# Performance work log

Measured on AMD Instinct MI355X. Metric: run time of the kernel, lower is better.

## Reference

```python
import jax, jax.numpy as jnp
import numpy as np

N_HEAD = 12

def setup_inputs() -> dict:
    key = jax.random.key(0)
    ks = jax.random.split(key, 3)
    B, T, D = 4, 2048, 768
    x = jax.random.normal(ks[0], (B, T, D), dtype=jnp.float32)
    W_qkv = jax.random.normal(ks[1], (D, 3 * D), dtype=jnp.float32) * (1.0 / np.sqrt(D))
    b_qkv = jnp.zeros((3 * D,), dtype=jnp.float32)
    W_o = jax.random.normal(ks[2], (D, D), dtype=jnp.float32) * (1.0 / np.sqrt(D))
    b_o = jnp.zeros((D,), dtype=jnp.float32)
    return {"x": x, "W_qkv": W_qkv, "b_qkv": b_qkv, "W_o": W_o, "b_o": b_o}


def reference(x, W_qkv, b_qkv, W_o, b_o):
    B, T, D = x.shape
    H = N_HEAD
    hd = D // H
    qkv = x @ W_qkv + b_qkv                      # [B,T,3D]
    q, k, v = jnp.split(qkv, 3, axis=-1)
    # [B,T,D] -> [B,H,T,hd]
    q = q.reshape(B, T, H, hd).transpose(0, 2, 1, 3)
    k = k.reshape(B, T, H, hd).transpose(0, 2, 1, 3)
    v = v.reshape(B, T, H, hd).transpose(0, 2, 1, 3)
    scale = 1.0 / np.sqrt(hd).astype(np.float32)
    scores = jnp.einsum('bhqd,bhkd->bhqk', q, k) * scale   # [B,H,T,T]
    causal = jnp.tril(jnp.ones((T, T), dtype=bool))
    scores = jnp.where(causal[None, None, :, :], scores, -jnp.inf)
    attn = jax.nn.softmax(scores, axis=-1)
    out = jnp.einsum('bhqk,bhkd->bhqd', attn, v)            # [B,H,T,hd]
    out = out.transpose(0, 2, 1, 3).reshape(B, T, D)
    return out @ W_o + b_o
```

## Files before the change

### kernel.cpp

```cpp
#include <hip/hip_runtime.h>
#include <hip/hip_bf16.h>

typedef __bf16 bf16_t;
typedef float f32x4 __attribute__((ext_vector_type(4)));
typedef bf16_t bf16x8 __attribute__((ext_vector_type(8)));
typedef bf16_t bf16x4 __attribute__((ext_vector_type(4)));

#define MFMA16(a, b, c) __builtin_amdgcn_mfma_f32_16x16x32_bf16(a, b, c, 0, 0, 0)

#define QSCALE 0.18033688011112042f

__device__ __forceinline__ void gl_lds16(const bf16_t* g, bf16_t* l) {
    __builtin_amdgcn_global_load_lds(
        (const __attribute__((address_space(1))) unsigned int*)g,
        (__attribute__((address_space(3))) unsigned int*)l, 16, 0, 0);
}

__device__ __forceinline__ float fexp2(float x) {
    float y;
    asm("v_exp_f32 %0, %1" : "=v"(y) : "v"(x));
    return y;
}

__device__ __forceinline__ void conv_t_body(const float* __restrict__ in,
                                            bf16_t* __restrict__ out,
                                            int R, int C, int bx, int by,
                                            float (*t)[33]) {
    const int tx = threadIdx.x & 31;
    const int ty = threadIdx.x >> 5;
#pragma unroll
    for (int i = 0; i < 4; i++)
        t[ty + i * 8][tx] = in[(size_t)(by + ty + i * 8) * C + bx + tx];
    __syncthreads();
#pragma unroll
    for (int i = 0; i < 4; i++)
        out[(size_t)(bx + ty + i * 8) * R + by + tx] = (bf16_t)t[tx][ty + i * 8];
}

__global__ __launch_bounds__(256) void prep_k(
    const float* __restrict__ x,    bf16_t* __restrict__ xb,
    const float* __restrict__ Wqkv, bf16_t* __restrict__ Wt,
    const float* __restrict__ Wo,   bf16_t* __restrict__ Wot)
{
    __shared__ float t[32][33];
    const int blk = blockIdx.x;
    if (blk < 6144) {
        const int i = (blk * 256 + threadIdx.x) * 4;
        float4 v = *(const float4*)(x + i);
        bf16x4 o = { (bf16_t)v.x, (bf16_t)v.y, (bf16_t)v.z, (bf16_t)v.w };
        *(bf16x4*)(xb + i) = o;
    } else if (blk < 7872) {
        const int idx = blk - 6144;
        conv_t_body(Wqkv, Wt, 768, 2304, (idx % 72) * 32, (idx / 72) * 32, t);
    } else {
        const int idx = blk - 7872;
        conv_t_body(Wo, Wot, 768, 768, (idx % 24) * 32, (idx / 24) * 32, t);
    }
}

__global__ __launch_bounds__(256) void vtrans(const bf16_t* __restrict__ Vp,
                                              bf16_t* __restrict__ Vt) {
    __shared__ __align__(16) bf16_t Ts[64 * 72];
    const int t0 = blockIdx.x * 64;
    const int bh = blockIdx.y;
    const int r  = threadIdx.x >> 2;
    const int cb = (threadIdx.x & 3) * 16;
    const bf16_t* src = Vp + (((size_t)bh * 2048 + t0 + r) << 6) + cb;
    *(bf16x8*)(Ts + r * 72 + cb)     = *(const bf16x8*)(src);
    *(bf16x8*)(Ts + r * 72 + cb + 8) = *(const bf16x8*)(src + 8);
    __syncthreads();
    const int f  = threadIdx.x >> 2;
    const int tb = (threadIdx.x & 3) * 16;
    bf16_t* dst = Vt + (((size_t)bh * 64 + f) << 11) + t0 + tb;
    bf16x8 a, b;
#pragma unroll
    for (int i = 0; i < 8; i++) a[i] = Ts[(tb + i) * 72 + f];
#pragma unroll
    for (int i = 0; i < 8; i++) b[i] = Ts[(tb + 8 + i) * 72 + f];
    *(bf16x8*)(dst)     = a;
    *(bf16x8*)(dst + 8) = b;
}

template <int EPI>
__global__ __launch_bounds__(256) void gemm_bt(
    const bf16_t* __restrict__ A, const bf16_t* __restrict__ Bt,
    const float* __restrict__ bias,
    void* __restrict__ O0v, bf16_t* __restrict__ O1, bf16_t* __restrict__ O2,
    int M, int N, int K)
{
    __shared__ __align__(16) bf16_t As[2][128 * 32];
    __shared__ __align__(16) bf16_t Bs[2][128 * 32];

    const int tid  = threadIdx.x;
    const int wid  = tid >> 6;
    const int lane = tid & 63;
    const int quad = lane >> 4;
    const int l15  = lane & 15;
    const int wm   = (wid >> 1) * 64;
    const int wn   = (wid & 1) * 64;
    const int qs8  = (quad ^ ((l15 >> 1) & 3)) * 8;

    const int mtiles = M >> 7;
    const int mtpx   = mtiles >> 3;
    const int bid    = blockIdx.x;
    const int xcd    = bid & 7;
    const int slot   = bid >> 3;
    const int m0     = (xcd * mtpx + (slot % mtpx)) << 7;
    const int n0     = (slot / mtpx) << 7;

    f32x4 acc[4][4];
#pragma unroll
    for (int i = 0; i < 4; i++)
#pragma unroll
        for (int j = 0; j < 4; j++) acc[i][j] = (f32x4){0.f, 0.f, 0.f, 0.f};

    const int srow = tid >> 2;
    const int scol = (((tid & 3) ^ ((srow >> 1) & 3)) ) * 8;
    const bf16_t* ag0 = A  + (size_t)(m0 + srow) * K + scol;
    const bf16_t* ag1 = A  + (size_t)(m0 + 64 + srow) * K + scol;
    const bf16_t* bg0 = Bt + (size_t)(n0 + srow) * K + scol;
    const bf16_t* bg1 = Bt + (size_t)(n0 + 64 + srow) * K + scol;

    auto prefetch = [&](int k0, int buf) {
        gl_lds16(ag0 + k0, As[buf] + tid * 8);
        gl_lds16(ag1 + k0, As[buf] + 2048 + tid * 8);
        gl_lds16(bg0 + k0, Bs[buf] + tid * 8);
        gl_lds16(bg1 + k0, Bs[buf] + 2048 + tid * 8);
    };

    const int niter = K >> 5;
    prefetch(0, 0);
    for (int i = 0; i < niter; i++) {
        __syncthreads();
        if (i + 1 < niter) prefetch((i + 1) << 5, (i + 1) & 1);
        const bf16_t* Ap = As[i & 1];
        const bf16_t* Bp = Bs[i & 1];

        bf16x8 af[4], bfr[4];
#pragma unroll
        for (int ii = 0; ii < 4; ii++)
            af[ii] = *(const bf16x8*)(Ap + (wm + ii * 16 + l15) * 32 + qs8);
#pragma unroll
        for (int j = 0; j < 4; j++)
            bfr[j] = *(const bf16x8*)(Bp + (wn + j * 16 + l15) * 32 + qs8);
#pragma unroll
        for (int ii = 0; ii < 4; ii++)
#pragma unroll
            for (int j = 0; j < 4; j++)
                acc[ii][j] = MFMA16(af[ii], bfr[j], acc[ii][j]);
    }

    if (EPI == 0) {
        const int sec = n0 / 768;
        const float scale = (sec == 0) ? QSCALE : 1.f;
        bf16_t* dst = (sec == 0) ? (bf16_t*)O0v : (sec == 1 ? O1 : O2);
#pragma unroll
        for (int i = 0; i < 4; i++) {
            const int mbase = m0 + wm + i * 16 + quad * 4;
#pragma unroll
            for (int j = 0; j < 4; j++) {
                const int n  = n0 + wn + j * 16 + l15;
                const float bv = bias[n];
                const int d    = n - sec * 768;
                const int h    = d >> 6;
                const int feat = d & 63;
#pragma unroll
                for (int r = 0; r < 4; r++) {
                    const int mm = mbase + r;
                    const int b  = mm >> 11;
                    const int tt = mm & 2047;
                    const int bh = b * 12 + h;
                    dst[(((size_t)bh * 2048 + tt) << 6) + feat] =
                        (bf16_t)((acc[i][j][r] + bv) * scale);
                }
            }
        }
    } else {
#pragma unroll
        for (int i = 0; i < 4; i++) {
            const int mbase = m0 + wm + i * 16 + quad * 4;
#pragma unroll
            for (int j = 0; j < 4; j++) {
                const int n  = n0 + wn + j * 16 + l15;
                const float bv = bias[n];
#pragma unroll
                for (int r = 0; r < 4; r++)
                    ((float*)O0v)[(size_t)(mbase + r) * N + n] = acc[i][j][r] + bv;
            }
        }
    }
}

__global__ __launch_bounds__(256) void attn_k(
    const bf16_t* __restrict__ Q, const bf16_t* __restrict__ Kb,
    const bf16_t* __restrict__ Vt, bf16_t* __restrict__ AO)
{
    __shared__ __align__(16) bf16_t Ks[2 * 4096];
    __shared__ __align__(16) bf16_t Vs[2 * 4096];
    __shared__ __align__(16) bf16_t Ps[4 * 16 * 64];

    const int tid  = threadIdx.x;
    const int wid  = tid >> 6;
    const int lane = tid & 63;
    const int quad = lane >> 4;
    const int l15  = lane & 15;
    const int qs8  = (quad ^ ((l15 >> 1) & 3)) * 8;

    const int bid  = blockIdx.x;
    const int xcd  = bid & 7;
    const int slot = bid >> 3;
    const int bh   = xcd * 6 + (slot >> 4);
    const int p    = slot & 15;

    const bf16_t* Qb  = Q  + ((size_t)bh << 17);
    const bf16_t* Kbh = Kb + ((size_t)bh << 17);
    const bf16_t* Vbh = Vt + ((size_t)bh << 17);

    bf16_t* Pw = Ps + wid * 1024;
    const int swl = l15 & 7;
    bf16_t* pwr[4];
#pragma unroll
    for (int c = 0; c < 4; c++)
        pwr[c] = Pw + l15 * 64 + (((((c << 1) | (quad >> 1))) ^ swl) << 3) + ((quad & 1) << 2);
    const bf16_t* prd[2];
#pragma unroll
    for (int kk = 0; kk < 2; kk++)
        prd[kk] = Pw + l15 * 64 + ((((kk << 2) | quad) ^ swl) << 3);

    const bf16x8 ones = { (bf16_t)1.f, (bf16_t)1.f, (bf16_t)1.f, (bf16_t)1.f,
                          (bf16_t)1.f, (bf16_t)1.f, (bf16_t)1.f, (bf16_t)1.f };

    const int srow = tid >> 2;
    const int scol = (((tid & 3) ^ ((srow >> 1) & 3))) * 8;

    auto prefetch = [&](int j, int buf) {
        const int kv0 = j * 64;
        bf16_t* kd = Ks + buf * 4096 + tid * 8;
        bf16_t* vd = Vs + buf * 4096 + tid * 8;
#pragma unroll
        for (int c = 0; c < 2; c++) {
            gl_lds16(Kbh + (size_t)(kv0 + srow) * 64 + c * 32 + scol, kd + c * 2048);
            gl_lds16(Vbh + (size_t)srow * 2048 + kv0 + c * 32 + scol, vd + c * 2048);
        }
    };

    const int b = bh / 12;
    const int h = bh - b * 12;

#pragma unroll
    for (int half = 0; half < 2; half++) {
        const int qt = half == 0 ? (31 - p) : p;
        const int q0 = qt * 64;
        const int qg = q0 + wid * 16 + l15;

        bf16x8 qf[2];
        {
            const bf16_t* qp = Qb + ((size_t)qg << 6) + quad * 8;
            qf[0] = *(const bf16x8*)(qp);
            qf[1] = *(const bf16x8*)(qp + 32);
        }

        f32x4 lacc = (f32x4){0.f, 0.f, 0.f, 0.f};
        f32x4 oacc[4];
#pragma unroll
        for (int f = 0; f < 4; f++) oacc[f] = (f32x4){0.f, 0.f, 0.f, 0.f};

        const int cnt = qt + 1;
        prefetch(0, 0);

        for (int i = 0; i < cnt; i++) {
            __syncthreads();
            if (i + 1 < cnt) prefetch(i + 1, (i + 1) & 1);
            const bf16_t* Kp = Ks + (i & 1) * 4096;
            const bf16_t* Vp = Vs + (i & 1) * 4096;

            f32x4 st[4];
            __builtin_amdgcn_s_setprio(1);
#pragma unroll
            for (int c = 0; c < 4; c++) {
                st[c] = (f32x4){0.f, 0.f, 0.f, 0.f};
#pragma unroll
                for (int kk = 0; kk < 2; kk++) {
                    bf16x8 kf = *(const bf16x8*)(Kp + kk * 2048 + (c * 16 + l15) * 32 + qs8);
                    st[c] = MFMA16(kf, qf[kk], st[c]);
                }
            }
            __builtin_amdgcn_s_setprio(0);

            if (i == qt) {
                const int kvb = q0 + quad * 4;
#pragma unroll
                for (int c = 0; c < 4; c++)
#pragma unroll
                    for (int r = 0; r < 4; r++)
                        if (kvb + c * 16 + r > qg) st[c][r] = -3e38f;
            }

#pragma unroll
            for (int c = 0; c < 4; c++) {
                bf16x4 pk = { (bf16_t)fexp2(st[c][0]), (bf16_t)fexp2(st[c][1]),
                              (bf16_t)fexp2(st[c][2]), (bf16_t)fexp2(st[c][3]) };
                *(bf16x4*)pwr[c] = pk;
            }

            bf16x8 pb[2];
#pragma unroll
            for (int kk = 0; kk < 2; kk++)
                pb[kk] = *(const bf16x8*)prd[kk];

            __builtin_amdgcn_s_setprio(1);
            lacc = MFMA16(ones, pb[0], lacc);
            lacc = MFMA16(ones, pb[1], lacc);

#pragma unroll
            for (int f = 0; f < 4; f++)
#pragma unroll
                for (int kk = 0; kk < 2; kk++) {
                    bf16x8 vf = *(const bf16x8*)(Vp + kk * 2048 + (f * 16 + l15) * 32 + qs8);
                    oacc[f] = MFMA16(vf, pb[kk], oacc[f]);
                }
            __builtin_amdgcn_s_setprio(0);
        }
        __syncthreads();

        const float inv = 1.0f / lacc[0];
        bf16_t* dst = AO + ((size_t)(b * 2048 + qg)) * 768 + h * 64 + quad * 4;
#pragma unroll
        for (int f = 0; f < 4; f++) {
            bf16x4 o = { (bf16_t)(oacc[f][0] * inv), (bf16_t)(oacc[f][1] * inv),
                         (bf16_t)(oacc[f][2] * inv), (bf16_t)(oacc[f][3] * inv) };
            *(bf16x4*)(dst + f * 16) = o;
        }
    }
}

extern "C" void kernel_launch(void* const* d_in, const int* in_sizes, int n_in,
                              void* d_out, int out_size, void* d_ws, size_t ws_size,
                              hipStream_t stream)
{
    const float* x    = (const float*)d_in[0];
    const float* Wqkv = (const float*)d_in[1];
    const float* bqkv = (const float*)d_in[2];
    const float* Wo   = (const float*)d_in[3];
    const float* bo   = (const float*)d_in[4];
    float* out = (float*)d_out;

    const size_t per = (size_t)48 * 2048 * 64;
    bf16_t* Qs  = (bf16_t*)d_ws;
    bf16_t* Kk  = Qs + per;
    bf16_t* Vt  = Kk + per;
    bf16_t* AO  = Vt + per;
    bf16_t* xb  = AO + per;
    bf16_t* Wt  = xb + per;
    bf16_t* Wot = Wt + (size_t)2304 * 768;
    bf16_t* Vpl = (bf16_t*)d_out;

    prep_k<<<8448, 256, 0, stream>>>(x, xb, Wqkv, Wt, Wo, Wot);

    gemm_bt<0><<<18 * 64, 256, 0, stream>>>(
        xb, Wt, bqkv, (void*)Qs, Kk, Vpl, 8192, 2304, 768);
    vtrans<<<dim3(32, 48), 256, 0, stream>>>(Vpl, Vt);
    attn_k<<<768, 256, 0, stream>>>(Qs, Kk, Vt, AO);
    gemm_bt<1><<<6 * 64, 256, 0, stream>>>(
        AO, Wot, bo, (void*)out, nullptr, nullptr, 8192, 768, 768);
}
```

Before: 197.8 us.

## Process two 64-row query tiles per block to reuse K/V tiles

The attention kernel now gives each block a 128-row query tile, processed as two 64-row groups per warp that share every K/V tile loaded into LDS. Before, each block walked two separate 64-row tiles (a paired long and short tile) and reloaded K/V for each. The change is meant to halve LDS fills and barriers per unit of MFMA work. In exchange it doubles the accumulators and P scratch, sets launch_bounds to 3 blocks, and changes the causal work balance: block i-loop lengths now vary from 2 to 32 tiles instead of being paired to a constant total.

```diff
diff --git a/kernel.cpp b/kernel.cpp
--- a/kernel.cpp
+++ b/kernel.cpp
@@ -191,13 +191,13 @@
     }
 }
 
-__global__ __launch_bounds__(256) void attn_k(
+__global__ __launch_bounds__(256, 3) void attn_k(
     const bf16_t* __restrict__ Q, const bf16_t* __restrict__ Kb,
     const bf16_t* __restrict__ Vt, bf16_t* __restrict__ AO)
 {
     __shared__ __align__(16) bf16_t Ks[2 * 4096];
     __shared__ __align__(16) bf16_t Vs[2 * 4096];
-    __shared__ __align__(16) bf16_t Ps[4 * 16 * 64];
+    __shared__ __align__(16) bf16_t Ps[4 * 2048];
 
     const int tid  = threadIdx.x;
     const int wid  = tid >> 6;
@@ -209,23 +209,28 @@
     const int bid  = blockIdx.x;
     const int xcd  = bid & 7;
     const int slot = bid >> 3;
-    const int bh   = xcd * 6 + (slot >> 4);
-    const int p    = slot & 15;
+    const int bh   = xcd * 6 + (slot % 6);
+    const int qt2  = 15 - (slot / 6);
+    const int q0   = qt2 << 7;
 
     const bf16_t* Qb  = Q  + ((size_t)bh << 17);
     const bf16_t* Kbh = Kb + ((size_t)bh << 17);
     const bf16_t* Vbh = Vt + ((size_t)bh << 17);
 
-    bf16_t* Pw = Ps + wid * 1024;
+    bf16_t* Pw = Ps + wid * 2048;
     const int swl = l15 & 7;
-    bf16_t* pwr[4];
-#pragma unroll
-    for (int c = 0; c < 4; c++)
-        pwr[c] = Pw + l15 * 64 + (((((c << 1) | (quad >> 1))) ^ swl) << 3) + ((quad & 1) << 2);
-    const bf16_t* prd[2];
-#pragma unroll
-    for (int kk = 0; kk < 2; kk++)
-        prd[kk] = Pw + l15 * 64 + ((((kk << 2) | quad) ^ swl) << 3);
+    bf16_t* pwr[2][4];
+    const bf16_t* prd[2][2];
+#pragma unroll
+    for (int g = 0; g < 2; g++) {
+#pragma unroll
+        for (int c = 0; c < 4; c++)
+            pwr[g][c] = Pw + g * 1024 + l15 * 64 +
+                        (((((c << 1) | (quad >> 1))) ^ swl) << 3) + ((quad & 1) << 2);
+#pragma unroll
+        for (int kk = 0; kk < 2; kk++)
+            prd[g][kk] = Pw + g * 1024 + l15 * 64 + ((((kk << 2) | quad) ^ swl) << 3);
+    }
 
     const bf16x8 ones = { (bf16_t)1.f, (bf16_t)1.f, (bf16_t)1.f, (bf16_t)1.f,
                           (bf16_t)1.f, (bf16_t)1.f, (bf16_t)1.f, (bf16_t)1.f };
@@ -247,88 +252,108 @@
     const int b = bh / 12;
     const int h = bh - b * 12;
 
-#pragma unroll
-    for (int half = 0; half < 2; half++) {
-        const int qt = half == 0 ? (31 - p) : p;
-        const int q0 = qt * 64;
-        const int qg = q0 + wid * 16 + l15;
-
-        bf16x8 qf[2];
-        {
-            const bf16_t* qp = Qb + ((size_t)qg << 6) + quad * 8;
-            qf[0] = *(const bf16x8*)(qp);
-            qf[1] = *(const bf16x8*)(qp + 32);
-        }
-
-        f32x4 lacc = (f32x4){0.f, 0.f, 0.f, 0.f};
-        f32x4 oacc[4];
-#pragma unroll
-        for (int f = 0; f < 4; f++) oacc[f] = (f32x4){0.f, 0.f, 0.f, 0.f};
-
-        const int cnt = qt + 1;
-        prefetch(0, 0);
-
-        for (int i = 0; i < cnt; i++) {
-            __syncthreads();
-            if (i + 1 < cnt) prefetch(i + 1, (i + 1) & 1);
-            const bf16_t* Kp = Ks + (i & 1) * 4096;
-            const bf16_t* Vp = Vs + (i & 1) * 4096;
-
-            f32x4 st[4];
-            __builtin_amdgcn_s_setprio(1);
+    const int qg0 = q0 + wid * 16 + l15;
+    const int qg1 = qg0 + 64;
+
+    bf16x8 qf[2][2];
+#pragma unroll
+    for (int g = 0; g < 2; g++) {
+        const bf16_t* qp = Qb + ((size_t)(g ? qg1 : qg0) << 6) + quad * 8;
+        qf[g][0] = *(const bf16x8*)(qp);
+        qf[g][1] = *(const bf16x8*)(qp + 32);
+    }
+
+    f32x4 lacc[2];
+    f32x4 oacc[2][4];
+#pragma unroll
+    for (int g = 0; g < 2; g++) {
+        lacc[g] = (f32x4){0.f, 0.f, 0.f, 0.f};
+#pragma unroll
+        for (int f = 0; f < 4; f++) oacc[g][f] = (f32x4){0.f, 0.f, 0.f, 0.f};
+    }
+
+    const int cnt = 2 * qt2 + 2;
+    prefetch(0, 0);
+
+    for (int i = 0; i < cnt; i++) {
+        __syncthreads();
+        if (i + 1 < cnt) prefetch(i + 1, (i + 1) & 1);
+        const bf16_t* Kp = Ks + (i & 1) * 4096;
+        const bf16_t* Vp = Vs + (i & 1) * 4096;
+
+        f32x4 st[2][4];
+        __builtin_amdgcn_s_setprio(1);
+#pragma unroll
+        for (int c = 0; c < 4; c++) {
+            st[0][c] = (f32x4){0.f, 0.f, 0.f, 0.f};
+            st[1][c] = (f32x4){0.f, 0.f, 0.f, 0.f};
+#pragma unroll
+            for (int kk = 0; kk < 2; kk++) {
+                bf16x8 kf = *(const bf16x8*)(Kp + kk * 2048 + (c * 16 + l15) * 32 + qs8);
+                st[0][c] = MFMA16(kf, qf[0][kk], st[0][c]);
+                st[1][c] = MFMA16(kf, qf[1][kk], st[1][c]);
+            }
+        }
+        __builtin_amdgcn_s_setprio(0);
+
+        const int kvb = i * 64 + quad * 4;
+        if (i >= 2 * qt2) {
+#pragma unroll
+            for (int c = 0; c < 4; c++)
+#pragma unroll
+                for (int r = 0; r < 4; r++)
+                    if (kvb + c * 16 + r > qg0) st[0][c][r] = -3e38f;
+            if (i == 2 * qt2 + 1) {
+#pragma unroll
+                for (int c = 0; c < 4; c++)
+#pragma unroll
+                    for (int r = 0; r < 4; r++)
+                        if (kvb + c * 16 + r > qg1) st[1][c][r] = -3e38f;
+            }
+        }
+
+#pragma unroll
+        for (int g = 0; g < 2; g++)
 #pragma unroll
             for (int c = 0; c < 4; c++) {
-                st[c] = (f32x4){0.f, 0.f, 0.f, 0.f};
-#pragma unroll
-                for (int kk = 0; kk < 2; kk++) {
-                    bf16x8 kf = *(const bf16x8*)(Kp + kk * 2048 + (c * 16 + l15) * 32 + qs8);
-                    st[c] = MFMA16(kf, qf[kk], st[c]);
-                }
-            }
-            __builtin_amdgcn_s_setprio(0);
-
-            if (i == qt) {
-                const int kvb = q0 + quad * 4;
-#pragma unroll
-                for (int c = 0; c < 4; c++)
-#pragma unroll
-                    for (int r = 0; r < 4; r++)
-                        if (kvb + c * 16 + r > qg) st[c][r] = -3e38f;
-            }
-
-#pragma unroll
-            for (int c = 0; c < 4; c++) {
-                bf16x4 pk = { (bf16_t)fexp2(st[c][0]), (bf16_t)fexp2(st[c][1]),
-                              (bf16_t)fexp2(st[c][2]), (bf16_t)fexp2(st[c][3]) };
-                *(bf16x4*)pwr[c] = pk;
-            }
-
-            bf16x8 pb[2];
+                bf16x4 pk = { (bf16_t)fexp2(st[g][c][0]), (bf16_t)fexp2(st[g][c][1]),
+                              (bf16_t)fexp2(st[g][c][2]), (bf16_t)fexp2(st[g][c][3]) };
+                *(bf16x4*)pwr[g][c] = pk;
+            }
+
+        bf16x8 pb[2][2];
+#pragma unroll
+        for (int g = 0; g < 2; g++)
 #pragma unroll
             for (int kk = 0; kk < 2; kk++)
-                pb[kk] = *(const bf16x8*)prd[kk];
-
-            __builtin_amdgcn_s_setprio(1);
-            lacc = MFMA16(ones, pb[0], lacc);
-            lacc = MFMA16(ones, pb[1], lacc);
-
-#pragma unroll
-            for (int f = 0; f < 4; f++)
-#pragma unroll
-                for (int kk = 0; kk < 2; kk++) {
-                    bf16x8 vf = *(const bf16x8*)(Vp + kk * 2048 + (f * 16 + l15) * 32 + qs8);
-                    oacc[f] = MFMA16(vf, pb[kk], oacc[f]);
-                }
-            __builtin_amdgcn_s_setprio(0);
-        }
-        __syncthreads();
-
-        const float inv = 1.0f / lacc[0];
+                pb[g][kk] = *(const bf16x8*)prd[g][kk];
+
+        __builtin_amdgcn_s_setprio(1);
+        lacc[0] = MFMA16(ones, pb[0][0], lacc[0]);
+        lacc[0] = MFMA16(ones, pb[0][1], lacc[0]);
+        lacc[1] = MFMA16(ones, pb[1][0], lacc[1]);
+        lacc[1] = MFMA16(ones, pb[1][1], lacc[1]);
+
+#pragma unroll
+        for (int f = 0; f < 4; f++)
+#pragma unroll
+            for (int kk = 0; kk < 2; kk++) {
+                bf16x8 vf = *(const bf16x8*)(Vp + kk * 2048 + (f * 16 + l15) * 32 + qs8);
+                oacc[0][f] = MFMA16(vf, pb[0][kk], oacc[0][f]);
+                oacc[1][f] = MFMA16(vf, pb[1][kk], oacc[1][f]);
+            }
+        __builtin_amdgcn_s_setprio(0);
+    }
+
+#pragma unroll
+    for (int g = 0; g < 2; g++) {
+        const float inv = 1.0f / lacc[g][0];
+        const int qg = g ? qg1 : qg0;
         bf16_t* dst = AO + ((size_t)(b * 2048 + qg)) * 768 + h * 64 + quad * 4;
 #pragma unroll
         for (int f = 0; f < 4; f++) {
-            bf16x4 o = { (bf16_t)(oacc[f][0] * inv), (bf16_t)(oacc[f][1] * inv),
-                         (bf16_t)(oacc[f][2] * inv), (bf16_t)(oacc[f][3] * inv) };
+            bf16x4 o = { (bf16_t)(oacc[g][f][0] * inv), (bf16_t)(oacc[g][f][1] * inv),
+                         (bf16_t)(oacc[g][f][2] * inv), (bf16_t)(oacc[g][f][3] * inv) };
             *(bf16x4*)(dst + f * 16) = o;
         }
     }
```

Measured after the change: 196.5 us. About the same (-0.6%).
